# Optimization experiments

Hardware: AMD Instinct MI355X
Metric: run time of the kernel (lower is better)

The kernel has to match this reference:

```python
import jax, jax.numpy as jnp
import numpy as np
import math

B, S, D, H = 4, 1024, 512, 8
DK = D // H
NEG = -1e32


def setup_inputs() -> dict:
    key = jax.random.key(0)
    ks = jax.random.split(key, 16)
    f = lambda k, shape: jax.random.normal(k, shape, dtype=jnp.float32)
    w = 1.0 / math.sqrt(D)  # xavier-ish scale
    return {
        'query_mean': f(ks[0], (B, S, D)),
        'query_cov': f(ks[1], (B, S, D)),
        'key_mean': f(ks[2], (B, S, D)),
        'key_cov': f(ks[3], (B, S, D)),
        'values_mean': f(ks[4], (B, S, D)),
        'values_cov': f(ks[5], (B, S, D)),
        'Wk_mean': f(ks[6], (D, D)) * w, 'bk_mean': jnp.zeros((D,), jnp.float32),
        'Wk_cov': f(ks[7], (D, D)) * w, 'bk_cov': jnp.zeros((D,), jnp.float32),
        'Wv_mean': f(ks[8], (D, D)) * w, 'bv_mean': jnp.zeros((D,), jnp.float32),
        'Wv_cov': f(ks[9], (D, D)) * w, 'bv_cov': jnp.zeros((D,), jnp.float32),
        'Wo_mean': f(ks[10], (D, D)) * w, 'bo_mean': jnp.zeros((D,), jnp.float32),
        'Wo_cov': f(ks[11], (D, D)) * w, 'bo_cov': jnp.zeros((D,), jnp.float32),
        'gammas': f(ks[12], (H, 1, 1)) * 0.1,
        'mask': jnp.tril(jnp.ones((1, 1, S, S), dtype=jnp.int32)),
    }


def _forward(query_mean, query_cov, key_mean, key_cov, values_mean, values_cov,
             Wk_mean, bk_mean, Wk_cov, bk_cov, Wv_mean, bv_mean, Wv_cov, bv_cov,
             Wo_mean, bo_mean, Wo_cov, bo_cov, gammas, mask):
    def heads(x, W, b):  # [B,S,D] -> [B,H,S,DK]
        return (x @ W + b).reshape(B, S, H, DK).transpose(0, 2, 1, 3)

    # kq_same=True: queries and keys share the k linears
    qm = heads(query_mean, Wk_mean, bk_mean)
    qc = heads(query_cov, Wk_cov, bk_cov)
    km = heads(key_mean, Wk_mean, bk_mean)
    kc = heads(key_cov, Wk_cov, bk_cov)
    vm = heads(values_mean, Wv_mean, bv_mean)
    vc = heads(values_cov, Wv_cov, bv_cov)

    inv = 1.0 / math.sqrt(DK)
    sm = jnp.einsum('bhqd,bhkd->bhqk', qm, km) * inv  # [B,H,S,S]
    sc = jnp.einsum('bhqd,bhkd->bhqk', qc, kc) * inv

    maskf = mask.astype(jnp.float32)
    # position_effect[i,j] = |j - i|
    pos = jnp.abs(jnp.arange(S)[None, :] - jnp.arange(S)[:, None]).astype(jnp.float32)[None, None]

    def dist_scores(s):
        p = jax.nn.softmax(jnp.where(mask == 0, NEG, s), axis=-1) * maskf
        cum = jnp.cumsum(p, axis=-1)
        tot = jnp.sum(p, axis=-1, keepdims=True)
        return jnp.sqrt(jnp.clip((tot - cum) * pos, 0.0, None))

    dm = jax.lax.stop_gradient(dist_scores(sm))  # torch no_grad + detach
    dc = jax.lax.stop_gradient(dist_scores(sc))

    gv = -jax.nn.softplus(gammas)[None]  # [1,H,1,1]
    em = jnp.clip(jnp.exp(dm * gv), 1e-5, 1e5)
    ec = jnp.clip(jnp.exp(dc * gv), 1e-5, 1e5)

    am = jax.nn.softmax(jnp.where(mask == 0, NEG, sm * em), axis=-1)
    ac = jax.nn.softmax(jnp.where(mask == 0, NEG, sc * ec), axis=-1)

    om = jnp.einsum('bhqk,bhkd->bhqd', am, vm).transpose(0, 2, 1, 3).reshape(B, S, D)
    oc = jnp.einsum('bhqk,bhkd->bhqd', ac, vc).transpose(0, 2, 1, 3).reshape(B, S, D)
    return om @ Wo_mean + bo_mean, oc @ Wo_cov + bo_cov


def reference(query_mean, query_cov, key_mean, key_cov, values_mean, values_cov,
              Wk_mean, bk_mean, Wk_cov, bk_cov, Wv_mean, bv_mean, Wv_cov, bv_cov,
              Wo_mean, bo_mean, Wo_cov, bo_cov, gammas, mask):
    return _forward(query_mean, query_cov, key_mean, key_cov, values_mean, values_cov,
                    Wk_mean, bk_mean, Wk_cov, bk_cov, Wv_mean, bv_mean, Wv_cov, bv_cov,
                    Wo_mean, bo_mean, Wo_cov, bo_cov, gammas, mask)
```

## Files before the change

kernel.cpp:

```cpp
#include <hip/hip_runtime.h>
#include <hip/hip_bf16.h>
#include <math.h>

constexpr int B_  = 4;
constexpr int S_  = 1024;
constexpr int D_  = 512;
constexpr int H_  = 8;
constexpr int DK_ = 64;
constexpr int MROWS_ = B_ * S_;
constexpr size_t SZ_ = (size_t)B_ * H_ * S_ * DK_;
constexpr size_t WSZ_ = (size_t)D_ * D_;

typedef __attribute__((ext_vector_type(8))) short bf16x8;
typedef __attribute__((ext_vector_type(4))) float f32x4;

__device__ __forceinline__ float bf2f(unsigned short u) {
  union { unsigned int u; float f; } v; v.u = (unsigned int)u << 16; return v.f;
}
__device__ __forceinline__ unsigned short f2bf(float f) {
  union { float f; unsigned int u; } v; v.f = f;
  unsigned int r = v.u + 0x7FFFu + ((v.u >> 16) & 1u);
  return (unsigned short)(r >> 16);
}

struct TpArgs { const float* W[4]; unsigned short* out[4]; };

__global__ __launch_bounds__(256) void wtrans(TpArgs a) {
  const int z = blockIdx.z;
  const float* __restrict__ W = a.W[z];
  unsigned short* __restrict__ out = a.out[z];
  __shared__ float T[64][65];
  const int tid = threadIdx.x;
  const int tx = blockIdx.x & 7, ty = blockIdx.x >> 3;
  const int k0 = ty * 64, n0 = tx * 64;
#pragma unroll
  for (int i = 0; i < 4; ++i) {
    const int idx = tid + i * 256;
    const int r = idx >> 4, c4 = (idx & 15) * 4;
    const float4 w = *(const float4*)&W[(size_t)(k0 + r) * D_ + n0 + c4];
    T[r][c4 + 0] = w.x; T[r][c4 + 1] = w.y; T[r][c4 + 2] = w.z; T[r][c4 + 3] = w.w;
  }
  __syncthreads();
#pragma unroll
  for (int i = 0; i < 4; ++i) {
    const int idx = tid + i * 256;
    const int n = idx >> 4, kc = (idx & 15) * 4;
    ushort4 pk;
    pk.x = f2bf(T[kc + 0][n]); pk.y = f2bf(T[kc + 1][n]);
    pk.z = f2bf(T[kc + 2][n]); pk.w = f2bf(T[kc + 3][n]);
    *(ushort4*)&out[(size_t)(n0 + n) * D_ + k0 + kc] = pk;
  }
}

struct ProjArgs {
  const float* A[6]; const unsigned short* Wt[6]; const float* bias[6];
  unsigned short* out[6]; int vmode[6];
};

__global__ __launch_bounds__(256) void proj_mfma(ProjArgs args) {
  const int z = blockIdx.z;
  const float* __restrict__ A = args.A[z];
  const unsigned short* __restrict__ Wt = args.Wt[z];
  const float* __restrict__ bias = args.bias[z];
  unsigned short* __restrict__ out = args.out[z];
  const int vmode = args.vmode[z];

  __shared__ unsigned short Abuf[128][40];
  __shared__ unsigned short Bbuf[128][40];
  const int tid = threadIdx.x, wv = tid >> 6, lane = tid & 63;
  const int quad = lane >> 4, l16 = lane & 15;
  const int wm = wv >> 1, wn = wv & 1;
  const int n0 = blockIdx.x * 128, m0 = blockIdx.y * 128;

  f32x4 acc[4][4];
#pragma unroll
  for (int i = 0; i < 4; ++i)
#pragma unroll
    for (int j = 0; j < 4; ++j) acc[i][j] = (f32x4){0.f, 0.f, 0.f, 0.f};

  for (int kt = 0; kt < 16; ++kt) {
    const int k0 = kt * 32;
    __syncthreads();
#pragma unroll
    for (int i = 0; i < 4; ++i) {
      const int idx = tid + i * 256;
      const int m = idx >> 3, c = idx & 7;
      const float4 av = *(const float4*)&A[(size_t)(m0 + m) * D_ + k0 + c * 4];
      ushort4 p;
      p.x = f2bf(av.x); p.y = f2bf(av.y); p.z = f2bf(av.z); p.w = f2bf(av.w);
      *(ushort4*)&Abuf[m][c * 4] = p;
    }
#pragma unroll
    for (int i = 0; i < 2; ++i) {
      const int idx = tid + i * 256;
      const int n = idx >> 2, c = idx & 3;
      *(uint4*)&Bbuf[n][c * 8] = *(const uint4*)&Wt[(size_t)(n0 + n) * D_ + k0 + c * 8];
    }
    __syncthreads();

    bf16x8 af[4], bfr[4];
#pragma unroll
    for (int i = 0; i < 4; ++i) af[i] = *(const bf16x8*)&Abuf[wm * 64 + i * 16 + l16][quad * 8];
#pragma unroll
    for (int j = 0; j < 4; ++j) bfr[j] = *(const bf16x8*)&Bbuf[wn * 64 + j * 16 + l16][quad * 8];
#pragma unroll
    for (int i = 0; i < 4; ++i)
#pragma unroll
      for (int j = 0; j < 4; ++j)
        acc[i][j] = __builtin_amdgcn_mfma_f32_16x16x32_bf16(af[i], bfr[j], acc[i][j], 0, 0, 0);
  }

#pragma unroll
  for (int j = 0; j < 4; ++j) {
    const int col = n0 + wn * 64 + j * 16 + l16;
    const float bv = bias[col];
    const int h = col >> 6, dk = col & 63;
#pragma unroll
    for (int i = 0; i < 4; ++i) {
      const int mbase = m0 + wm * 64 + i * 16 + quad * 4;
      const int b = mbase >> 10;
      if (!vmode) {
#pragma unroll
        for (int r = 0; r < 4; ++r) {
          const int s = (mbase + r) & 1023;
          out[(((size_t)b * H_ + h) * S_ + s) * DK_ + dk] = f2bf(acc[i][j][r] + bv);
        }
      } else {
        const int s = mbase & 1023;
        ushort4 pk;
        pk.x = f2bf(acc[i][j][0] + bv); pk.y = f2bf(acc[i][j][1] + bv);
        pk.z = f2bf(acc[i][j][2] + bv); pk.w = f2bf(acc[i][j][3] + bv);
        *(ushort4*)&out[(((size_t)b * H_ + h) * DK_ + dk) * S_ + s] = pk;
      }
    }
  }
}

struct OutArgs {
  const unsigned short* A[2]; const unsigned short* Wt[2];
  const float* bias[2]; float* out[2];
};

__global__ __launch_bounds__(256) void out_mfma(OutArgs args) {
  const int z = blockIdx.z;
  const unsigned short* __restrict__ A = args.A[z];
  const unsigned short* __restrict__ Wt = args.Wt[z];
  const float* __restrict__ bias = args.bias[z];
  float* __restrict__ out = args.out[z];

  __shared__ unsigned short Abuf[128][40];
  __shared__ unsigned short Bbuf[128][40];
  const int tid = threadIdx.x, wv = tid >> 6, lane = tid & 63;
  const int quad = lane >> 4, l16 = lane & 15;
  const int wm = wv >> 1, wn = wv & 1;
  const int n0 = blockIdx.x * 128, m0 = blockIdx.y * 128;

  f32x4 acc[4][4];
#pragma unroll
  for (int i = 0; i < 4; ++i)
#pragma unroll
    for (int j = 0; j < 4; ++j) acc[i][j] = (f32x4){0.f, 0.f, 0.f, 0.f};

  for (int kt = 0; kt < 16; ++kt) {
    const int k0 = kt * 32;
    __syncthreads();
#pragma unroll
    for (int i = 0; i < 2; ++i) {
      const int idx = tid + i * 256;
      const int m = idx >> 2, c = idx & 3;
      *(uint4*)&Abuf[m][c * 8] = *(const uint4*)&A[(size_t)(m0 + m) * D_ + k0 + c * 8];
    }
#pragma unroll
    for (int i = 0; i < 2; ++i) {
      const int idx = tid + i * 256;
      const int n = idx >> 2, c = idx & 3;
      *(uint4*)&Bbuf[n][c * 8] = *(const uint4*)&Wt[(size_t)(n0 + n) * D_ + k0 + c * 8];
    }
    __syncthreads();

    bf16x8 af[4], bfr[4];
#pragma unroll
    for (int i = 0; i < 4; ++i) af[i] = *(const bf16x8*)&Abuf[wm * 64 + i * 16 + l16][quad * 8];
#pragma unroll
    for (int j = 0; j < 4; ++j) bfr[j] = *(const bf16x8*)&Bbuf[wn * 64 + j * 16 + l16][quad * 8];
#pragma unroll
    for (int i = 0; i < 4; ++i)
#pragma unroll
      for (int j = 0; j < 4; ++j)
        acc[i][j] = __builtin_amdgcn_mfma_f32_16x16x32_bf16(af[i], bfr[j], acc[i][j], 0, 0, 0);
  }

#pragma unroll
  for (int j = 0; j < 4; ++j) {
    const int col = n0 + wn * 64 + j * 16 + l16;
    const float bv = bias[col];
#pragma unroll
    for (int i = 0; i < 4; ++i) {
      const int mbase = m0 + wm * 64 + i * 16 + quad * 4;
#pragma unroll
      for (int r = 0; r < 4; ++r)
        out[(size_t)(mbase + r) * D_ + col] = acc[i][j][r] + bv;
    }
  }
}

__global__ __launch_bounds__(256) void attn_mfma(
    const unsigned short* __restrict__ qkv, const float* __restrict__ gammas,
    unsigned short* __restrict__ Obase)
{
  __shared__ unsigned short Qs[64][72];
  __shared__ unsigned short Ks[64][72];
  __shared__ unsigned short Vts[64][72];
  __shared__ unsigned short Ps[4][16][72];

  const int tid = threadIdx.x;
  const int wv = tid >> 6, lane = tid & 63, quad = lane >> 4, l16 = lane & 15;
  const int bh = blockIdx.x;
  const int qt = 15 - blockIdx.y;
  const int ch = blockIdx.z;
  const int q0 = qt << 6;
  const int b = bh >> 3, h = bh & 7;

  const unsigned short* Q  = qkv + (size_t)ch * 3 * SZ_ + (size_t)bh * S_ * DK_;
  const unsigned short* K  = qkv + (size_t)ch * 3 * SZ_ + SZ_ + (size_t)bh * S_ * DK_;
  const unsigned short* Vt = qkv + (size_t)ch * 3 * SZ_ + 2 * SZ_ + (size_t)bh * (size_t)DK_ * S_;
  unsigned short* O = Obase + (size_t)ch * SZ_;

  const float g = gammas[h];
  const float gv = -(fmaxf(g, 0.f) + log1pf(__expf(-fabsf(g))));

#pragma unroll
  for (int it = 0; it < 2; ++it) {
    const int c = tid + it * 256, r = c >> 3, cc = c & 7;
    *(uint4*)&Qs[r][cc * 8] = *(const uint4*)&Q[(size_t)(q0 + r) * DK_ + cc * 8];
  }
  __syncthreads();
  const bf16x8 qf0 = *(const bf16x8*)&Qs[wv * 16 + l16][quad * 8];
  const bf16x8 qf1 = *(const bf16x8*)&Qs[wv * 16 + l16][32 + quad * 8];

  const int myrow = q0 + wv * 16 + quad * 4;

  float m1[4] = {-1e30f, -1e30f, -1e30f, -1e30f};
  float T[4]  = {0.f, 0.f, 0.f, 0.f};

  for (int kt = 0; kt <= qt; ++kt) {
    __syncthreads();
#pragma unroll
    for (int it = 0; it < 2; ++it) {
      const int c = tid + it * 256, r = c >> 3, cc = c & 7;
      *(uint4*)&Ks[r][cc * 8] = *(const uint4*)&K[(size_t)(kt * 64 + r) * DK_ + cc * 8];
    }
    __syncthreads();

    f32x4 sa[4];
#pragma unroll
    for (int cb = 0; cb < 4; ++cb) {
      const bf16x8 kf0 = *(const bf16x8*)&Ks[cb * 16 + l16][quad * 8];
      const bf16x8 kf1 = *(const bf16x8*)&Ks[cb * 16 + l16][32 + quad * 8];
      f32x4 a = {0.f, 0.f, 0.f, 0.f};
      a = __builtin_amdgcn_mfma_f32_16x16x32_bf16(qf0, kf0, a, 0, 0, 0);
      a = __builtin_amdgcn_mfma_f32_16x16x32_bf16(qf1, kf1, a, 0, 0, 0);
      sa[cb] = a;
    }
    const bool diag = (kt == qt);
#pragma unroll
    for (int cb = 0; cb < 4; ++cb)
#pragma unroll
      for (int r = 0; r < 4; ++r) {
        float s = sa[cb][r] * 0.125f;
        if (diag && (kt * 64 + cb * 16 + l16) > (myrow + r)) s = -1e30f;
        sa[cb][r] = s;
      }
#pragma unroll
    for (int r = 0; r < 4; ++r) {
      float mx = fmaxf(fmaxf(sa[0][r], sa[1][r]), fmaxf(sa[2][r], sa[3][r]));
      mx = fmaxf(mx, __shfl_xor(mx, 1, 64)); mx = fmaxf(mx, __shfl_xor(mx, 2, 64));
      mx = fmaxf(mx, __shfl_xor(mx, 4, 64)); mx = fmaxf(mx, __shfl_xor(mx, 8, 64));
      const float mn = fmaxf(m1[r], mx);
      float sum = __expf(sa[0][r] - mn) + __expf(sa[1][r] - mn) +
                  __expf(sa[2][r] - mn) + __expf(sa[3][r] - mn);
      sum += __shfl_xor(sum, 1, 64); sum += __shfl_xor(sum, 2, 64);
      sum += __shfl_xor(sum, 4, 64); sum += __shfl_xor(sum, 8, 64);
      T[r] = T[r] * __expf(m1[r] - mn) + sum;
      m1[r] = mn;
    }
  }

  float invT[4];
#pragma unroll
  for (int r = 0; r < 4; ++r) invT[r] = 1.f / T[r];

  float carry[4] = {0.f, 0.f, 0.f, 0.f};
  float m2[4] = {-1e30f, -1e30f, -1e30f, -1e30f};
  float l2[4] = {0.f, 0.f, 0.f, 0.f};
  f32x4 oacc[4];
#pragma unroll
  for (int cb = 0; cb < 4; ++cb) oacc[cb] = (f32x4){0.f, 0.f, 0.f, 0.f};

  for (int kt = 0; kt <= qt; ++kt) {
    __syncthreads();
#pragma unroll
    for (int it = 0; it < 2; ++it) {
      const int c = tid + it * 256, r = c >> 3, cc = c & 7;
      *(uint4*)&Ks[r][cc * 8]  = *(const uint4*)&K[(size_t)(kt * 64 + r) * DK_ + cc * 8];
      *(uint4*)&Vts[r][cc * 8] = *(const uint4*)&Vt[(size_t)r * S_ + kt * 64 + cc * 8];
    }
    __syncthreads();

    f32x4 sa[4];
#pragma unroll
    for (int cb = 0; cb < 4; ++cb) {
      const bf16x8 kf0 = *(const bf16x8*)&Ks[cb * 16 + l16][quad * 8];
      const bf16x8 kf1 = *(const bf16x8*)&Ks[cb * 16 + l16][32 + quad * 8];
      f32x4 a = {0.f, 0.f, 0.f, 0.f};
      a = __builtin_amdgcn_mfma_f32_16x16x32_bf16(qf0, kf0, a, 0, 0, 0);
      a = __builtin_amdgcn_mfma_f32_16x16x32_bf16(qf1, kf1, a, 0, 0, 0);
      sa[cb] = a;
    }
    const bool diag = (kt == qt);
#pragma unroll
    for (int cb = 0; cb < 4; ++cb)
#pragma unroll
      for (int r = 0; r < 4; ++r) {
        float s = sa[cb][r] * 0.125f;
        if (diag && (kt * 64 + cb * 16 + l16) > (myrow + r)) s = -1e30f;
        sa[cb][r] = s;
      }

#pragma unroll
    for (int r = 0; r < 4; ++r) {
      float p0 = __expf(sa[0][r] - m1[r]) * invT[r];
      float p1 = __expf(sa[1][r] - m1[r]) * invT[r];
      float p2 = __expf(sa[2][r] - m1[r]) * invT[r];
      float p3 = __expf(sa[3][r] - m1[r]) * invT[r];
      float v0 = p0, v1 = p1, v2 = p2, v3 = p3;
#pragma unroll
      for (int off = 1; off < 16; off <<= 1) {
        const float t0 = __shfl_up(v0, off, 64);
        const float t1 = __shfl_up(v1, off, 64);
        const float t2 = __shfl_up(v2, off, 64);
        const float t3 = __shfl_up(v3, off, 64);
        if (l16 >= off) { v0 += t0; v1 += t1; v2 += t2; v3 += t3; }
      }
      const int lastlane = (lane & 48) | 15;
      const float tt0 = __shfl(v0, lastlane, 64);
      const float tt1 = __shfl(v1, lastlane, 64);
      const float tt2 = __shfl(v2, lastlane, 64);
      const float tt3 = __shfl(v3, lastlane, 64);
      const float base = carry[r];
      const float cum0 = base + v0;
      const float cum1 = base + tt0 + v1;
      const float cum2 = base + tt0 + tt1 + v2;
      const float cum3 = base + tt0 + tt1 + tt2 + v3;
      carry[r] = base + tt0 + tt1 + tt2 + tt3;

      const float rowf = (float)(myrow + r);
      const float k0f = (float)(kt * 64 + l16);
      {
        float pos = rowf - (k0f + 0.f);
        float dd = sqrtf(fmaxf((1.f - cum0) * pos, 0.f));
        float e = fminf(fmaxf(__expf(dd * gv), 1e-5f), 1e5f);
        sa[0][r] = sa[0][r] * e;
        pos = rowf - (k0f + 16.f);
        dd = sqrtf(fmaxf((1.f - cum1) * pos, 0.f));
        e = fminf(fmaxf(__expf(dd * gv), 1e-5f), 1e5f);
        sa[1][r] = sa[1][r] * e;
        pos = rowf - (k0f + 32.f);
        dd = sqrtf(fmaxf((1.f - cum2) * pos, 0.f));
        e = fminf(fmaxf(__expf(dd * gv), 1e-5f), 1e5f);
        sa[2][r] = sa[2][r] * e;
        pos = rowf - (k0f + 48.f);
        dd = sqrtf(fmaxf((1.f - cum3) * pos, 0.f));
        e = fminf(fmaxf(__expf(dd * gv), 1e-5f), 1e5f);
        sa[3][r] = sa[3][r] * e;
      }

      float mx = fmaxf(fmaxf(sa[0][r], sa[1][r]), fmaxf(sa[2][r], sa[3][r]));
      mx = fmaxf(mx, __shfl_xor(mx, 1, 64)); mx = fmaxf(mx, __shfl_xor(mx, 2, 64));
      mx = fmaxf(mx, __shfl_xor(mx, 4, 64)); mx = fmaxf(mx, __shfl_xor(mx, 8, 64));
      const float mn = fmaxf(m2[r], mx);
      const float al = __expf(m2[r] - mn);
      m2[r] = mn;
      const float w0 = __expf(sa[0][r] - mn);
      const float w1 = __expf(sa[1][r] - mn);
      const float w2 = __expf(sa[2][r] - mn);
      const float w3 = __expf(sa[3][r] - mn);
      float sum = w0 + w1 + w2 + w3;
      sum += __shfl_xor(sum, 1, 64); sum += __shfl_xor(sum, 2, 64);
      sum += __shfl_xor(sum, 4, 64); sum += __shfl_xor(sum, 8, 64);
      l2[r] = l2[r] * al + sum;
      oacc[0][r] *= al; oacc[1][r] *= al; oacc[2][r] *= al; oacc[3][r] *= al;
      const int prow = quad * 4 + r;
      Ps[wv][prow][ 0 + l16] = f2bf(w0);
      Ps[wv][prow][16 + l16] = f2bf(w1);
      Ps[wv][prow][32 + l16] = f2bf(w2);
      Ps[wv][prow][48 + l16] = f2bf(w3);
    }
    asm volatile("s_waitcnt lgkmcnt(0)" ::: "memory");

    const bf16x8 pf0 = *(const bf16x8*)&Ps[wv][l16][quad * 8];
    const bf16x8 pf1 = *(const bf16x8*)&Ps[wv][l16][32 + quad * 8];
#pragma unroll
    for (int cb = 0; cb < 4; ++cb) {
      const bf16x8 vf0 = *(const bf16x8*)&Vts[cb * 16 + l16][quad * 8];
      const bf16x8 vf1 = *(const bf16x8*)&Vts[cb * 16 + l16][32 + quad * 8];
      oacc[cb] = __builtin_amdgcn_mfma_f32_16x16x32_bf16(pf0, vf0, oacc[cb], 0, 0, 0);
      oacc[cb] = __builtin_amdgcn_mfma_f32_16x16x32_bf16(pf1, vf1, oacc[cb], 0, 0, 0);
    }
  }

#pragma unroll
  for (int r = 0; r < 4; ++r) {
    const float inv = 1.f / l2[r];
    const int srow = myrow + r;
    const size_t base = ((size_t)b * S_ + srow) * D_ + h * DK_;
    O[base +  0 + l16] = f2bf(oacc[0][r] * inv);
    O[base + 16 + l16] = f2bf(oacc[1][r] * inv);
    O[base + 32 + l16] = f2bf(oacc[2][r] * inv);
    O[base + 48 + l16] = f2bf(oacc[3][r] * inv);
  }
}

extern "C" void kernel_launch(void* const* d_in, const int* in_sizes, int n_in,
                              void* d_out, int out_size, void* d_ws, size_t ws_size,
                              hipStream_t stream) {
  const float* query_mean  = (const float*)d_in[0];
  const float* query_cov   = (const float*)d_in[1];
  const float* key_mean    = (const float*)d_in[2];
  const float* key_cov     = (const float*)d_in[3];
  const float* values_mean = (const float*)d_in[4];
  const float* values_cov  = (const float*)d_in[5];
  const float* Wk_mean = (const float*)d_in[6];
  const float* bk_mean = (const float*)d_in[7];
  const float* Wk_cov  = (const float*)d_in[8];
  const float* bk_cov  = (const float*)d_in[9];
  const float* Wv_mean = (const float*)d_in[10];
  const float* bv_mean = (const float*)d_in[11];
  const float* Wv_cov  = (const float*)d_in[12];
  const float* bv_cov  = (const float*)d_in[13];
  const float* Wo_mean = (const float*)d_in[14];
  const float* bo_mean = (const float*)d_in[15];
  const float* Wo_cov  = (const float*)d_in[16];
  const float* bo_cov  = (const float*)d_in[17];
  const float* gammas  = (const float*)d_in[18];

  unsigned short* qkv  = (unsigned short*)d_ws;
  unsigned short* obuf = qkv + 6 * SZ_;
  unsigned short* Wt4  = (unsigned short*)d_out;
  unsigned short* Wot  = qkv + 2 * SZ_;
  float* out = (float*)d_out;

  TpArgs t1;
  t1.W[0] = Wk_mean; t1.W[1] = Wv_mean; t1.W[2] = Wk_cov; t1.W[3] = Wv_cov;
  for (int i = 0; i < 4; ++i) t1.out[i] = Wt4 + (size_t)i * WSZ_;
  wtrans<<<dim3(64, 1, 4), 256, 0, stream>>>(t1);

  ProjArgs pa;
  const float* pA[6] = {query_mean, key_mean, values_mean, query_cov, key_cov, values_cov};
  const int   wIdx[6] = {0, 0, 1, 2, 2, 3};
  const float* pb[6] = {bk_mean, bk_mean, bv_mean, bk_cov, bk_cov, bv_cov};
  const int pv[6] = {0, 0, 1, 0, 0, 1};
  for (int i = 0; i < 6; ++i) {
    pa.A[i] = pA[i]; pa.Wt[i] = Wt4 + (size_t)wIdx[i] * WSZ_; pa.bias[i] = pb[i];
    pa.out[i] = qkv + (size_t)i * SZ_; pa.vmode[i] = pv[i];
  }
  proj_mfma<<<dim3(4, 32, 6), 256, 0, stream>>>(pa);

  attn_mfma<<<dim3(32, 16, 2), 256, 0, stream>>>(qkv, gammas, obuf);

  TpArgs t2;
  t2.W[0] = Wo_mean; t2.W[1] = Wo_cov; t2.W[2] = Wo_mean; t2.W[3] = Wo_cov;
  t2.out[0] = Wot; t2.out[1] = Wot + WSZ_; t2.out[2] = Wot; t2.out[3] = Wot + WSZ_;
  wtrans<<<dim3(64, 1, 2), 256, 0, stream>>>(t2);

  OutArgs oa;
  oa.A[0] = obuf;        oa.A[1] = obuf + SZ_;
  oa.Wt[0] = Wot;        oa.Wt[1] = Wot + WSZ_;
  oa.bias[0] = bo_mean;  oa.bias[1] = bo_cov;
  oa.out[0] = out;       oa.out[1] = out + (size_t)MROWS_ * D_;
  out_mfma<<<dim3(4, 32, 2), 256, 0, stream>>>(oa);
}
```

Before: 298.1 us.

## Restructure causal attention kernel: paired query tiles, direct global loads, no-max softmax, DPP scans

```diff
diff --git a/kernel.cpp b/kernel.cpp
--- a/kernel.cpp
+++ b/kernel.cpp
@@ -21,6 +21,30 @@
   union { float f; unsigned int u; } v; v.f = f;
   unsigned int r = v.u + 0x7FFFu + ((v.u >> 16) & 1u);
   return (unsigned short)(r >> 16);
+}
+
+template <int CTRL>
+__device__ __forceinline__ float dpp_mov_f(float x) {
+  return __builtin_bit_cast(float,
+      __builtin_amdgcn_update_dpp(0, __builtin_bit_cast(int, x), CTRL, 0xF, 0xF, true));
+}
+__device__ __forceinline__ float scan16(float v) {
+  v += dpp_mov_f<0x111>(v);
+  v += dpp_mov_f<0x112>(v);
+  v += dpp_mov_f<0x114>(v);
+  v += dpp_mov_f<0x118>(v);
+  return v;
+}
+__device__ __forceinline__ float red16(float v) {
+  v += dpp_mov_f<0x128>(v);
+  v += dpp_mov_f<0x124>(v);
+  v += dpp_mov_f<0x122>(v);
+  v += dpp_mov_f<0x121>(v);
+  return v;
+}
+__device__ __forceinline__ float bcast15(float v) {
+  return __builtin_bit_cast(float,
+      __builtin_amdgcn_ds_swizzle(__builtin_bit_cast(int, v), 0x01F0));
 }
 
 struct TpArgs { const float* W[4]; unsigned short* out[4]; };
@@ -204,20 +228,19 @@
   }
 }
 
-__global__ __launch_bounds__(256) void attn_mfma(
+__global__ __launch_bounds__(512) void attn_mfma(
     const unsigned short* __restrict__ qkv, const float* __restrict__ gammas,
     unsigned short* __restrict__ Obase)
 {
-  __shared__ unsigned short Qs[64][72];
-  __shared__ unsigned short Ks[64][72];
-  __shared__ unsigned short Vts[64][72];
-  __shared__ unsigned short Ps[4][16][72];
+  __shared__ unsigned short Ps[8][16][72];
 
   const int tid = threadIdx.x;
-  const int wv = tid >> 6, lane = tid & 63, quad = lane >> 4, l16 = lane & 15;
+  const int w = tid >> 6, lane = tid & 63, quad = lane >> 4, l16 = lane & 15;
   const int bh = blockIdx.x;
-  const int qt = 15 - blockIdx.y;
+  const int pair = blockIdx.y;
   const int ch = blockIdx.z;
+  const int qt = (w < 4) ? (15 - pair) : pair;
+  const int wq = w & 3;
   const int q0 = qt << 6;
   const int b = bh >> 3, h = bh & 7;
 
@@ -229,189 +252,135 @@
   const float g = gammas[h];
   const float gv = -(fmaxf(g, 0.f) + log1pf(__expf(-fabsf(g))));
 
-#pragma unroll
-  for (int it = 0; it < 2; ++it) {
-    const int c = tid + it * 256, r = c >> 3, cc = c & 7;
-    *(uint4*)&Qs[r][cc * 8] = *(const uint4*)&Q[(size_t)(q0 + r) * DK_ + cc * 8];
-  }
-  __syncthreads();
-  const bf16x8 qf0 = *(const bf16x8*)&Qs[wv * 16 + l16][quad * 8];
-  const bf16x8 qf1 = *(const bf16x8*)&Qs[wv * 16 + l16][32 + quad * 8];
-
-  const int myrow = q0 + wv * 16 + quad * 4;
-
-  float m1[4] = {-1e30f, -1e30f, -1e30f, -1e30f};
-  float T[4]  = {0.f, 0.f, 0.f, 0.f};
-
+  const unsigned short* Qrow = Q + (size_t)(q0 + wq * 16 + l16) * DK_;
+  const bf16x8 qf0 = *(const bf16x8*)(Qrow + quad * 8);
+  const bf16x8 qf1 = *(const bf16x8*)(Qrow + 32 + quad * 8);
+  const int myrow = q0 + wq * 16 + quad * 4;
+
+  float Tacc[4] = {0.f, 0.f, 0.f, 0.f};
   for (int kt = 0; kt <= qt; ++kt) {
-    __syncthreads();
-#pragma unroll
-    for (int it = 0; it < 2; ++it) {
-      const int c = tid + it * 256, r = c >> 3, cc = c & 7;
-      *(uint4*)&Ks[r][cc * 8] = *(const uint4*)&K[(size_t)(kt * 64 + r) * DK_ + cc * 8];
-    }
-    __syncthreads();
-
     f32x4 sa[4];
 #pragma unroll
     for (int cb = 0; cb < 4; ++cb) {
-      const bf16x8 kf0 = *(const bf16x8*)&Ks[cb * 16 + l16][quad * 8];
-      const bf16x8 kf1 = *(const bf16x8*)&Ks[cb * 16 + l16][32 + quad * 8];
+      const unsigned short* Kr = K + (size_t)(kt * 64 + cb * 16 + l16) * DK_;
+      const bf16x8 kf0 = *(const bf16x8*)(Kr + quad * 8);
+      const bf16x8 kf1 = *(const bf16x8*)(Kr + 32 + quad * 8);
       f32x4 a = {0.f, 0.f, 0.f, 0.f};
       a = __builtin_amdgcn_mfma_f32_16x16x32_bf16(qf0, kf0, a, 0, 0, 0);
       a = __builtin_amdgcn_mfma_f32_16x16x32_bf16(qf1, kf1, a, 0, 0, 0);
       sa[cb] = a;
     }
-    const bool diag = (kt == qt);
-#pragma unroll
-    for (int cb = 0; cb < 4; ++cb)
-#pragma unroll
-      for (int r = 0; r < 4; ++r) {
-        float s = sa[cb][r] * 0.125f;
-        if (diag && (kt * 64 + cb * 16 + l16) > (myrow + r)) s = -1e30f;
-        sa[cb][r] = s;
-      }
-#pragma unroll
-    for (int r = 0; r < 4; ++r) {
-      float mx = fmaxf(fmaxf(sa[0][r], sa[1][r]), fmaxf(sa[2][r], sa[3][r]));
-      mx = fmaxf(mx, __shfl_xor(mx, 1, 64)); mx = fmaxf(mx, __shfl_xor(mx, 2, 64));
-      mx = fmaxf(mx, __shfl_xor(mx, 4, 64)); mx = fmaxf(mx, __shfl_xor(mx, 8, 64));
-      const float mn = fmaxf(m1[r], mx);
-      float sum = __expf(sa[0][r] - mn) + __expf(sa[1][r] - mn) +
-                  __expf(sa[2][r] - mn) + __expf(sa[3][r] - mn);
-      sum += __shfl_xor(sum, 1, 64); sum += __shfl_xor(sum, 2, 64);
-      sum += __shfl_xor(sum, 4, 64); sum += __shfl_xor(sum, 8, 64);
-      T[r] = T[r] * __expf(m1[r] - mn) + sum;
-      m1[r] = mn;
-    }
-  }
-
+    if (kt == qt) {
+#pragma unroll
+      for (int cb = 0; cb < 4; ++cb)
+#pragma unroll
+        for (int r = 0; r < 4; ++r) {
+          float e = __expf(sa[cb][r] * 0.125f);
+          if ((kt * 64 + cb * 16 + l16) > (myrow + r)) e = 0.f;
+          Tacc[r] += e;
+        }
+    } else {
+#pragma unroll
+      for (int cb = 0; cb < 4; ++cb)
+#pragma unroll
+        for (int r = 0; r < 4; ++r)
+          Tacc[r] += __expf(sa[cb][r] * 0.125f);
+    }
+  }
   float invT[4];
 #pragma unroll
-  for (int r = 0; r < 4; ++r) invT[r] = 1.f / T[r];
+  for (int r = 0; r < 4; ++r) invT[r] = 1.f / red16(Tacc[r]);
 
   float carry[4] = {0.f, 0.f, 0.f, 0.f};
-  float m2[4] = {-1e30f, -1e30f, -1e30f, -1e30f};
-  float l2[4] = {0.f, 0.f, 0.f, 0.f};
+  float l2a[4] = {0.f, 0.f, 0.f, 0.f};
   f32x4 oacc[4];
 #pragma unroll
   for (int cb = 0; cb < 4; ++cb) oacc[cb] = (f32x4){0.f, 0.f, 0.f, 0.f};
 
   for (int kt = 0; kt <= qt; ++kt) {
-    __syncthreads();
-#pragma unroll
-    for (int it = 0; it < 2; ++it) {
-      const int c = tid + it * 256, r = c >> 3, cc = c & 7;
-      *(uint4*)&Ks[r][cc * 8]  = *(const uint4*)&K[(size_t)(kt * 64 + r) * DK_ + cc * 8];
-      *(uint4*)&Vts[r][cc * 8] = *(const uint4*)&Vt[(size_t)r * S_ + kt * 64 + cc * 8];
-    }
-    __syncthreads();
+    bf16x8 vf0[4], vf1[4];
+#pragma unroll
+    for (int cb = 0; cb < 4; ++cb) {
+      const unsigned short* Vr = Vt + (size_t)(cb * 16 + l16) * S_ + kt * 64;
+      vf0[cb] = *(const bf16x8*)(Vr + quad * 8);
+      vf1[cb] = *(const bf16x8*)(Vr + 32 + quad * 8);
+    }
 
     f32x4 sa[4];
 #pragma unroll
     for (int cb = 0; cb < 4; ++cb) {
-      const bf16x8 kf0 = *(const bf16x8*)&Ks[cb * 16 + l16][quad * 8];
-      const bf16x8 kf1 = *(const bf16x8*)&Ks[cb * 16 + l16][32 + quad * 8];
+      const unsigned short* Kr = K + (size_t)(kt * 64 + cb * 16 + l16) * DK_;
+      const bf16x8 kf0 = *(const bf16x8*)(Kr + quad * 8);
+      const bf16x8 kf1 = *(const bf16x8*)(Kr + 32 + quad * 8);
       f32x4 a = {0.f, 0.f, 0.f, 0.f};
       a = __builtin_amdgcn_mfma_f32_16x16x32_bf16(qf0, kf0, a, 0, 0, 0);
       a = __builtin_amdgcn_mfma_f32_16x16x32_bf16(qf1, kf1, a, 0, 0, 0);
       sa[cb] = a;
     }
-    const bool diag = (kt == qt);
 #pragma unroll
     for (int cb = 0; cb < 4; ++cb)
 #pragma unroll
-      for (int r = 0; r < 4; ++r) {
-        float s = sa[cb][r] * 0.125f;
-        if (diag && (kt * 64 + cb * 16 + l16) > (myrow + r)) s = -1e30f;
-        sa[cb][r] = s;
+      for (int r = 0; r < 4; ++r) sa[cb][r] *= 0.125f;
+    if (kt == qt) {
+#pragma unroll
+      for (int cb = 0; cb < 4; ++cb)
+#pragma unroll
+        for (int r = 0; r < 4; ++r)
+          if ((kt * 64 + cb * 16 + l16) > (myrow + r)) sa[cb][r] = -1e30f;
+    }
+
+#pragma unroll
+    for (int r = 0; r < 4; ++r) {
+      float v0 = scan16(__expf(sa[0][r]));
+      float v1 = scan16(__expf(sa[1][r]));
+      float v2 = scan16(__expf(sa[2][r]));
+      float v3 = scan16(__expf(sa[3][r]));
+      const float tt0 = bcast15(v0), tt1 = bcast15(v1);
+      const float tt2 = bcast15(v2), tt3 = bcast15(v3);
+      const float base = carry[r];
+      const float p01 = tt0 + tt1, p012 = p01 + tt2;
+      const float cum0 = (base + v0) * invT[r];
+      const float cum1 = (base + tt0 + v1) * invT[r];
+      const float cum2 = (base + p01 + v2) * invT[r];
+      const float cum3 = (base + p012 + v3) * invT[r];
+      carry[r] = base + p012 + tt3;
+
+      const float bpos = (float)(myrow + r) - (float)(kt * 64 + l16);
+      float st0, st1, st2, st3;
+      {
+        float dd = sqrtf(fmaxf((1.f - cum0) * bpos, 0.f));
+        st0 = sa[0][r] * fminf(fmaxf(__expf(dd * gv), 1e-5f), 1e5f);
+        dd = sqrtf(fmaxf((1.f - cum1) * (bpos - 16.f), 0.f));
+        st1 = sa[1][r] * fminf(fmaxf(__expf(dd * gv), 1e-5f), 1e5f);
+        dd = sqrtf(fmaxf((1.f - cum2) * (bpos - 32.f), 0.f));
+        st2 = sa[2][r] * fminf(fmaxf(__expf(dd * gv), 1e-5f), 1e5f);
+        dd = sqrtf(fmaxf((1.f - cum3) * (bpos - 48.f), 0.f));
+        st3 = sa[3][r] * fminf(fmaxf(__expf(dd * gv), 1e-5f), 1e5f);
       }
 
-#pragma unroll
-    for (int r = 0; r < 4; ++r) {
-      float p0 = __expf(sa[0][r] - m1[r]) * invT[r];
-      float p1 = __expf(sa[1][r] - m1[r]) * invT[r];
-      float p2 = __expf(sa[2][r] - m1[r]) * invT[r];
-      float p3 = __expf(sa[3][r] - m1[r]) * invT[r];
-      float v0 = p0, v1 = p1, v2 = p2, v3 = p3;
-#pragma unroll
-      for (int off = 1; off < 16; off <<= 1) {
-        const float t0 = __shfl_up(v0, off, 64);
-        const float t1 = __shfl_up(v1, off, 64);
-        const float t2 = __shfl_up(v2, off, 64);
-        const float t3 = __shfl_up(v3, off, 64);
-        if (l16 >= off) { v0 += t0; v1 += t1; v2 += t2; v3 += t3; }
-      }
-      const int lastlane = (lane & 48) | 15;
-      const float tt0 = __shfl(v0, lastlane, 64);
-      const float tt1 = __shfl(v1, lastlane, 64);
-      const float tt2 = __shfl(v2, lastlane, 64);
-      const float tt3 = __shfl(v3, lastlane, 64);
-      const float base = carry[r];
-      const float cum0 = base + v0;
-      const float cum1 = base + tt0 + v1;
-      const float cum2 = base + tt0 + tt1 + v2;
-      const float cum3 = base + tt0 + tt1 + tt2 + v3;
-      carry[r] = base + tt0 + tt1 + tt2 + tt3;
-
-      const float rowf = (float)(myrow + r);
-      const float k0f = (float)(kt * 64 + l16);
-      {
-        float pos = rowf - (k0f + 0.f);
-        float dd = sqrtf(fmaxf((1.f - cum0) * pos, 0.f));
-        float e = fminf(fmaxf(__expf(dd * gv), 1e-5f), 1e5f);
-        sa[0][r] = sa[0][r] * e;
-        pos = rowf - (k0f + 16.f);
-        dd = sqrtf(fmaxf((1.f - cum1) * pos, 0.f));
-        e = fminf(fmaxf(__expf(dd * gv), 1e-5f), 1e5f);
-        sa[1][r] = sa[1][r] * e;
-        pos = rowf - (k0f + 32.f);
-        dd = sqrtf(fmaxf((1.f - cum2) * pos, 0.f));
-        e = fminf(fmaxf(__expf(dd * gv), 1e-5f), 1e5f);
-        sa[2][r] = sa[2][r] * e;
-        pos = rowf - (k0f + 48.f);
-        dd = sqrtf(fmaxf((1.f - cum3) * pos, 0.f));
-        e = fminf(fmaxf(__expf(dd * gv), 1e-5f), 1e5f);
-        sa[3][r] = sa[3][r] * e;
-      }
-
-      float mx = fmaxf(fmaxf(sa[0][r], sa[1][r]), fmaxf(sa[2][r], sa[3][r]));
-      mx = fmaxf(mx, __shfl_xor(mx, 1, 64)); mx = fmaxf(mx, __shfl_xor(mx, 2, 64));
-      mx = fmaxf(mx, __shfl_xor(mx, 4, 64)); mx = fmaxf(mx, __shfl_xor(mx, 8, 64));
-      const float mn = fmaxf(m2[r], mx);
-      const float al = __expf(m2[r] - mn);
-      m2[r] = mn;
-      const float w0 = __expf(sa[0][r] - mn);
-      const float w1 = __expf(sa[1][r] - mn);
-      const float w2 = __expf(sa[2][r] - mn);
-      const float w3 = __expf(sa[3][r] - mn);
-      float sum = w0 + w1 + w2 + w3;
-      sum += __shfl_xor(sum, 1, 64); sum += __shfl_xor(sum, 2, 64);
-      sum += __shfl_xor(sum, 4, 64); sum += __shfl_xor(sum, 8, 64);
-      l2[r] = l2[r] * al + sum;
-      oacc[0][r] *= al; oacc[1][r] *= al; oacc[2][r] *= al; oacc[3][r] *= al;
+      const float w0 = __expf(st0), w1 = __expf(st1);
+      const float w2 = __expf(st2), w3 = __expf(st3);
+      l2a[r] += (w0 + w1) + (w2 + w3);
       const int prow = quad * 4 + r;
-      Ps[wv][prow][ 0 + l16] = f2bf(w0);
-      Ps[wv][prow][16 + l16] = f2bf(w1);
-      Ps[wv][prow][32 + l16] = f2bf(w2);
-      Ps[wv][prow][48 + l16] = f2bf(w3);
+      Ps[w][prow][ 0 + l16] = f2bf(w0);
+      Ps[w][prow][16 + l16] = f2bf(w1);
+      Ps[w][prow][32 + l16] = f2bf(w2);
+      Ps[w][prow][48 + l16] = f2bf(w3);
     }
     asm volatile("s_waitcnt lgkmcnt(0)" ::: "memory");
 
-    const bf16x8 pf0 = *(const bf16x8*)&Ps[wv][l16][quad * 8];
-    const bf16x8 pf1 = *(const bf16x8*)&Ps[wv][l16][32 + quad * 8];
+    const bf16x8 pf0 = *(const bf16x8*)&Ps[w][l16][quad * 8];
+    const bf16x8 pf1 = *(const bf16x8*)&Ps[w][l16][32 + quad * 8];
 #pragma unroll
     for (int cb = 0; cb < 4; ++cb) {
-      const bf16x8 vf0 = *(const bf16x8*)&Vts[cb * 16 + l16][quad * 8];
-      const bf16x8 vf1 = *(const bf16x8*)&Vts[cb * 16 + l16][32 + quad * 8];
-      oacc[cb] = __builtin_amdgcn_mfma_f32_16x16x32_bf16(pf0, vf0, oacc[cb], 0, 0, 0);
-      oacc[cb] = __builtin_amdgcn_mfma_f32_16x16x32_bf16(pf1, vf1, oacc[cb], 0, 0, 0);
+      oacc[cb] = __builtin_amdgcn_mfma_f32_16x16x32_bf16(pf0, vf0[cb], oacc[cb], 0, 0, 0);
+      oacc[cb] = __builtin_amdgcn_mfma_f32_16x16x32_bf16(pf1, vf1[cb], oacc[cb], 0, 0, 0);
     }
   }
 
 #pragma unroll
   for (int r = 0; r < 4; ++r) {
-    const float inv = 1.f / l2[r];
+    const float inv = 1.f / red16(l2a[r]);
     const int srow = myrow + r;
     const size_t base = ((size_t)b * S_ + srow) * D_ + h * DK_;
     O[base +  0 + l16] = f2bf(oacc[0][r] * inv);
@@ -466,7 +435,7 @@
   }
   proj_mfma<<<dim3(4, 32, 6), 256, 0, stream>>>(pa);
 
-  attn_mfma<<<dim3(32, 16, 2), 256, 0, stream>>>(qkv, gammas, obuf);
+  attn_mfma<<<dim3(32, 8, 2), 512, 0, stream>>>(qkv, gammas, obuf);
 
   TpArgs t2;
   t2.W[0] = Wo_mean; t2.W[1] = Wo_cov; t2.W[2] = Wo_mean; t2.W[3] = Wo_cov;
```

New measurement: 271.4 us. 1.1x faster.
